# Optimization experiments

Hardware: AMD Instinct MI355X
Metric: run time of the kernel (lower is better)

The kernel has to match this reference:

```python
import jax, jax.numpy as jnp
import numpy as np
import math

SAMPLING_FACTOR = 5


def setup_inputs() -> dict:
    key = jax.random.key(0)
    kq, kk, kv, ki = jax.random.split(key, 4)
    B, L_Q, L_K, d = 8, 4096, 4096, 64
    # U_part = min(5 * L_Q * ceil(log1p(L_K)), L_K) = 4096 for these sizes
    U_part = min(SAMPLING_FACTOR * L_Q * math.ceil(math.log1p(L_K)), L_K)
    q = jax.random.normal(kq, (B, L_Q, d), dtype=jnp.float32)
    K = jax.random.normal(kk, (B, L_K, d), dtype=jnp.float32)
    V = jax.random.normal(kv, (B, L_K, d), dtype=jnp.float32)
    index_sample = jax.random.randint(ki, (U_part,), 0, L_K)  # random key sample (torch.randint)
    return {"q": q, "K": K, "V": V, "index_sample": index_sample}


def reference(q, K, V, index_sample):
    B, L_Q, d = q.shape
    L_K = K.shape[1]
    log_L_Q = math.ceil(math.log1p(L_Q))
    u = min(SAMPLING_FACTOR * log_L_Q, L_Q)  # number of selected queries (45 here)

    # Random key sampling (indices shared across batch)
    K_sample = K[:, index_sample, :]                       # [B, U_part, d]
    # Q @ K_sample^T
    Q_K_sample = jnp.einsum('bqd,bud->bqu', q, K_sample)   # [B, L_Q, U_part]
    # Sparsity measure M = max - sum/L_K
    M = Q_K_sample.max(axis=-1) - Q_K_sample.sum(axis=-1) / L_K  # [B, L_Q]
    # Source uses topk(..., largest=False): pick queries with SMALLEST M (kept faithfully)
    _, M_top = jax.lax.top_k(-M, u)                        # [B, u]
    # Gather the selected queries
    Q_reduce = jnp.take_along_axis(q, M_top[:, :, None], axis=1)  # [B, u, d]
    # Full attention over all keys for the selected queries
    attn_scores = jnp.einsum('bud,bkd->buk', Q_reduce, K) / math.sqrt(d)  # [B, u, L_K]
    attn_probs = jax.nn.softmax(attn_scores, axis=-1)
    attn_output = jnp.einsum('buk,bkd->bud', attn_probs, V)  # [B, u, d]
    return attn_output, attn_scores
```

## Files before the change

kernel.cpp:

```cpp
#include <hip/hip_runtime.h>
#include <hip/hip_bf16.h>
#include <math.h>

#define BB 8
#define LQ 4096
#define LK 4096
#define DD 64
#define UU 45
#define CCAP 256
#define CUMTHR 96
#define ECH 32
#define PCH 32
#define MCG 4
#define GCH 32

typedef __bf16 bf16x8 __attribute__((ext_vector_type(8)));
typedef unsigned short ushort8 __attribute__((ext_vector_type(8)));
typedef float f32x4 __attribute__((ext_vector_type(4)));

__device__ inline unsigned short f2bf(float x) {
    unsigned u = __builtin_bit_cast(unsigned, x);
    return (unsigned short)((u + 0x7FFF + ((u >> 16) & 1)) >> 16);
}

__device__ inline void gl_lds16(const void* g, void* l) {
    __builtin_amdgcn_global_load_lds(
        (const __attribute__((address_space(1))) unsigned int*)g,
        (__attribute__((address_space(3))) unsigned int*)l, 16, 0, 0);
}

__global__ __launch_bounds__(256) void k_gatherK(const float* __restrict__ K,
                                                 const int* __restrict__ idx,
                                                 int Upart,
                                                 unsigned short* __restrict__ Kg,
                                                 double* __restrict__ part) {
    int b = blockIdx.y;
    int chunk = blockIdx.x;
    int u0 = chunk * 128;
    int t = threadIdx.x;
    int pt = t & 7;

    double acc[8] = {0,0,0,0,0,0,0,0};
    #pragma unroll
    for (int i = 0; i < 4; ++i) {
        int lin = i * 256 + t;
        int u = u0 + (lin >> 3);
        if (u < Upart) {
            int kr = idx[u];
            const float* src = &K[((size_t)b * LK + kr) * DD + pt * 8];
            float4 v0 = *(const float4*)src;
            float4 v1 = *(const float4*)(src + 4);
            ushort8 pk;
            pk[0]=f2bf(v0.x); pk[1]=f2bf(v0.y); pk[2]=f2bf(v0.z); pk[3]=f2bf(v0.w);
            pk[4]=f2bf(v1.x); pk[5]=f2bf(v1.y); pk[6]=f2bf(v1.z); pk[7]=f2bf(v1.w);
            *(ushort8*)&Kg[((size_t)b * 4096 + u) * 64 + pt * 8] = pk;
            acc[0] += (double)v0.x; acc[1] += (double)v0.y;
            acc[2] += (double)v0.z; acc[3] += (double)v0.w;
            acc[4] += (double)v1.x; acc[5] += (double)v1.y;
            acc[6] += (double)v1.z; acc[7] += (double)v1.w;
        }
    }
    __shared__ double sred[32][64];
    int rg = t >> 3;
    #pragma unroll
    for (int j = 0; j < 8; ++j) sred[rg][pt * 8 + j] = acc[j];
    __syncthreads();
    if (t < 64) {
        double s = 0.0;
        #pragma unroll
        for (int r = 0; r < 32; ++r) s += sred[r][t];
        part[((size_t)(b * GCH + chunk)) * 64 + t] = s;
    }
}

__global__ __launch_bounds__(256) void k_mfmaM(const float* __restrict__ Q,
                                               const unsigned short* __restrict__ Kg,
                                               float* __restrict__ maxpart) {
    int bx = blockIdx.x, cg = blockIdx.y, b = blockIdx.z;
    int t = threadIdx.x;
    int lane = t & 63, w = t >> 6;
    int row0 = bx * 256;

    __shared__ unsigned short smem[16384];

    for (int i = 0; i < 8; ++i) {
        int u = i * 256 + t;
        int r = u >> 3, s = u & 7;
        int c = s ^ (r & 7);
        const float* src = &Q[((size_t)b * LQ + row0 + r) * DD + c * 8];
        float4 v0 = *(const float4*)src;
        float4 v1 = *(const float4*)(src + 4);
        ushort8 pk;
        pk[0]=f2bf(v0.x); pk[1]=f2bf(v0.y); pk[2]=f2bf(v0.z); pk[3]=f2bf(v0.w);
        pk[4]=f2bf(v1.x); pk[5]=f2bf(v1.y); pk[6]=f2bf(v1.z); pk[7]=f2bf(v1.w);
        *(ushort8*)&smem[r * 64 + s * 8] = pk;
    }
    __syncthreads();

    bf16x8 afr[4][2];
    #pragma unroll
    for (int rf = 0; rf < 4; ++rf)
        #pragma unroll
        for (int kh = 0; kh < 2; ++kh) {
            int r = w * 64 + rf * 16 + (lane & 15);
            int slot = (kh * 4 + (lane >> 4)) ^ (r & 7);
            afr[rf][kh] = __builtin_bit_cast(bf16x8, *(const ushort8*)&smem[r * 64 + slot * 8]);
        }
    __syncthreads();

    int krl = lane >> 3;
    int kc8 = (lane & 7) ^ (krl & 7);
    const unsigned short* kgb = Kg + ((size_t)b * 4096 + cg * 1024) * 64;

    #define STAGE_K(buf, tile)                                                  \
        {                                                                       \
            _Pragma("unroll")                                                   \
            for (int i_ = 0; i_ < 4; ++i_) {                                    \
                int seg_ = w * 4 + i_;                                          \
                const unsigned short* g_ =                                      \
                    kgb + ((size_t)((tile) * 128 + seg_ * 8 + krl)) * 64 + kc8 * 8; \
                gl_lds16(g_, &smem[(buf) * 8192 + seg_ * 512]);                 \
            }                                                                   \
        }

    STAGE_K(0, 0)
    __syncthreads();

    float rowmax[4][4];
    #pragma unroll
    for (int rf = 0; rf < 4; ++rf)
        #pragma unroll
        for (int g = 0; g < 4; ++g) rowmax[rf][g] = -INFINITY;

    for (int tile = 0; tile < 8; ++tile) {
        int cur = tile & 1;
        if (tile < 7) STAGE_K(cur ^ 1, tile + 1)

        #pragma unroll
        for (int cf = 0; cf < 8; ++cf) {
            f32x4 acc[4];
            #pragma unroll
            for (int rf = 0; rf < 4; ++rf) acc[rf] = (f32x4){0.f, 0.f, 0.f, 0.f};
            #pragma unroll
            for (int kh = 0; kh < 2; ++kh) {
                int ccol = cf * 16 + (lane & 15);
                int slot = (kh * 4 + (lane >> 4)) ^ (ccol & 7);
                bf16x8 bfr = __builtin_bit_cast(bf16x8,
                    *(const ushort8*)&smem[cur * 8192 + ccol * 64 + slot * 8]);
                #pragma unroll
                for (int rf = 0; rf < 4; ++rf)
                    acc[rf] = __builtin_amdgcn_mfma_f32_16x16x32_bf16(afr[rf][kh], bfr, acc[rf], 0, 0, 0);
            }
            #pragma unroll
            for (int rf = 0; rf < 4; ++rf)
                #pragma unroll
                for (int g = 0; g < 4; ++g)
                    rowmax[rf][g] = fmaxf(rowmax[rf][g], acc[rf][g]);
        }
        __syncthreads();
    }

    #pragma unroll
    for (int rf = 0; rf < 4; ++rf)
        #pragma unroll
        for (int g = 0; g < 4; ++g) {
            float m = rowmax[rf][g];
            m = fmaxf(m, __shfl_xor(m, 1));
            m = fmaxf(m, __shfl_xor(m, 2));
            m = fmaxf(m, __shfl_xor(m, 4));
            m = fmaxf(m, __shfl_xor(m, 8));
            if ((lane & 15) == 0) {
                int row = row0 + w * 64 + rf * 16 + (lane >> 4) * 4 + g;
                maxpart[((size_t)(b * MCG + cg)) * LQ + row] = m;
            }
        }
}

__global__ __launch_bounds__(256) void k_meanmerge(const float* __restrict__ Q,
                                                   const double* __restrict__ part,
                                                   int nch,
                                                   const float* __restrict__ maxpart,
                                                   double* __restrict__ mt,
                                                   float* __restrict__ Map) {
    int b = blockIdx.y;
    int t = threadIdx.x;
    int r = blockIdx.x * 256 + t;
    __shared__ double sK[64];
    if (t < 64) {
        double s = 0.0;
        for (int ch = 0; ch < nch; ++ch)
            s += part[((size_t)(b * GCH + ch)) * 64 + t];
        sK[t] = s;
    }
    __syncthreads();
    const float* qr = &Q[((size_t)b * LQ + r) * DD];
    double a0 = 0, a1 = 0, a2 = 0, a3 = 0;
    #pragma unroll
    for (int d = 0; d < 64; d += 4) {
        a0 += (double)qr[d + 0] * sK[d + 0];
        a1 += (double)qr[d + 1] * sK[d + 1];
        a2 += (double)qr[d + 2] * sK[d + 2];
        a3 += (double)qr[d + 3] * sK[d + 3];
    }
    double m = ((a0 + a1) + (a2 + a3)) / (double)LK;
    mt[(size_t)b * LQ + r] = m;
    float mx = fmaxf(fmaxf(maxpart[((size_t)(b * MCG + 0)) * LQ + r],
                           maxpart[((size_t)(b * MCG + 1)) * LQ + r]),
                     fmaxf(maxpart[((size_t)(b * MCG + 2)) * LQ + r],
                           maxpart[((size_t)(b * MCG + 3)) * LQ + r]));
    Map[(size_t)b * LQ + r] = mx - (float)m;
}

__global__ __launch_bounds__(1024) void k_select(const float* __restrict__ Map,
                                                 int* __restrict__ cand,
                                                 int* __restrict__ cand_count) {
    int b = blockIdx.x;
    int t = threadIdx.x;
    __shared__ float mv[LQ];
    __shared__ int hist[1024];
    __shared__ int seg[256];
    __shared__ float wmin[16], wmax[16];
    __shared__ float s_min, s_max;
    __shared__ int s_bstar, s_cnt;

    float lmin = INFINITY, lmax = -INFINITY;
    for (int i = t; i < LQ; i += 1024) {
        float v = Map[(size_t)b * LQ + i];
        mv[i] = v;
        lmin = fminf(lmin, v);
        lmax = fmaxf(lmax, v);
    }
    #pragma unroll
    for (int m = 1; m < 64; m <<= 1) {
        lmin = fminf(lmin, __shfl_xor(lmin, m));
        lmax = fmaxf(lmax, __shfl_xor(lmax, m));
    }
    int wid = t >> 6;
    if ((t & 63) == 0) { wmin[wid] = lmin; wmax[wid] = lmax; }
    if (t < 1024) hist[t] = 0;
    __syncthreads();
    if (t == 0) {
        float mn = wmin[0], mx = wmax[0];
        #pragma unroll
        for (int i = 1; i < 16; ++i) { mn = fminf(mn, wmin[i]); mx = fmaxf(mx, wmax[i]); }
        s_min = mn; s_max = mx;
        s_cnt = 0;
        s_bstar = 1023;
    }
    __syncthreads();
    float vmin = s_min;
    float w = (s_max - vmin) * (1.0f / 1024.0f);
    if (w <= 0.f) w = 1e-30f;
    float inv = 1.0f / w;
    for (int i = t; i < LQ; i += 1024) {
        int bin = (int)((mv[i] - vmin) * inv);
        bin = min(max(bin, 0), 1023);
        atomicAdd(&hist[bin], 1);
    }
    __syncthreads();
    int h0 = 0, h1 = 0, h2 = 0, h3 = 0;
    if (t < 256) {
        h0 = hist[t * 4 + 0]; h1 = hist[t * 4 + 1];
        h2 = hist[t * 4 + 2]; h3 = hist[t * 4 + 3];
        seg[t] = h0 + h1 + h2 + h3;
    }
    __syncthreads();
    for (int off = 1; off < 256; off <<= 1) {
        int v = 0, add = 0;
        if (t < 256) { v = seg[t]; add = (t >= off) ? seg[t - off] : 0; }
        __syncthreads();
        if (t < 256) seg[t] = v + add;
        __syncthreads();
    }
    if (t < 256) {
        int prev = (t == 0) ? 0 : seg[t - 1];
        if (seg[t] >= CUMTHR && prev < CUMTHR) {
            int cum = prev, bs = t * 4 + 3;
            if (cum + h0 >= CUMTHR) bs = t * 4;
            else if (cum + h0 + h1 >= CUMTHR) bs = t * 4 + 1;
            else if (cum + h0 + h1 + h2 >= CUMTHR) bs = t * 4 + 2;
            s_bstar = bs;
        }
    }
    __syncthreads();
    int bstar = s_bstar;
    for (int i = t; i < LQ; i += 1024) {
        int bin = (int)((mv[i] - vmin) * inv);
        bin = min(max(bin, 0), 1023);
        if (bin <= bstar) {
            int p = atomicAdd(&s_cnt, 1);
            if (p < CCAP) cand[b * CCAP + p] = i;
        }
    }
    __syncthreads();
    if (t == 0) cand_count[b] = min(s_cnt, CCAP);
}

__global__ __launch_bounds__(256, 1) void k_exact(const float* __restrict__ Q,
                                                  const float* __restrict__ K,
                                                  const int* __restrict__ idx,
                                                  const int* __restrict__ cand,
                                                  const int* __restrict__ cand_count,
                                                  float* __restrict__ exactpart) {
    int kc = blockIdx.x;
    int b  = blockIdx.y;
    int t = threadIdx.x;
    int lane = t & 63, w = t >> 6;
    __shared__ float Ks[128 * 64];
    __shared__ float wmx[4][CCAP];

    #pragma unroll
    for (int p = 0; p < 8; ++p) {
        int row = p * 16 + (t >> 4);
        int c4 = t & 15;
        int kr = idx[kc * 128 + row];
        *(float4*)&Ks[row * 64 + c4 * 4] =
            *(const float4*)&K[((size_t)b * LK + kr) * DD + c4 * 4];
    }

    int count = cand_count[b];
    int npass = (count + 127) >> 7;
    __syncthreads();

    for (int pass = 0; pass < npass; ++pass) {
        int s0 = pass * 128 + lane;
        int s1 = s0 + 64;
        float4 q0[16], q1[16];
        {
            float4 z = {0.f, 0.f, 0.f, 0.f};
            if (s0 < count) {
                const float4* qp = (const float4*)&Q[((size_t)b * LQ + cand[b * CCAP + s0]) * DD];
                #pragma unroll
                for (int i = 0; i < 16; ++i) q0[i] = qp[i];
            } else {
                #pragma unroll
                for (int i = 0; i < 16; ++i) q0[i] = z;
            }
            if (s1 < count) {
                const float4* qp = (const float4*)&Q[((size_t)b * LQ + cand[b * CCAP + s1]) * DD];
                #pragma unroll
                for (int i = 0; i < 16; ++i) q1[i] = qp[i];
            } else {
                #pragma unroll
                for (int i = 0; i < 16; ++i) q1[i] = z;
            }
        }

        float m0 = -INFINITY, m1 = -INFINITY;
        int kbeg = w * 32;
        for (int k = kbeg; k < kbeg + 32; ++k) {
            const float4* kr4 = (const float4*)&Ks[k * 64];
            float a0=0.f,a1=0.f,a2=0.f,a3=0.f;
            float c0=0.f,c1=0.f,c2=0.f,c3=0.f;
            #pragma unroll
            for (int i = 0; i < 16; i += 4) {
                float4 kv0 = kr4[i+0], kv1 = kr4[i+1], kv2 = kr4[i+2], kv3 = kr4[i+3];
                a0 = fmaf(q0[i+0].x, kv0.x, a0); a0 = fmaf(q0[i+0].y, kv0.y, a0);
                a0 = fmaf(q0[i+0].z, kv0.z, a0); a0 = fmaf(q0[i+0].w, kv0.w, a0);
                a1 = fmaf(q0[i+1].x, kv1.x, a1); a1 = fmaf(q0[i+1].y, kv1.y, a1);
                a1 = fmaf(q0[i+1].z, kv1.z, a1); a1 = fmaf(q0[i+1].w, kv1.w, a1);
                a2 = fmaf(q0[i+2].x, kv2.x, a2); a2 = fmaf(q0[i+2].y, kv2.y, a2);
                a2 = fmaf(q0[i+2].z, kv2.z, a2); a2 = fmaf(q0[i+2].w, kv2.w, a2);
                a3 = fmaf(q0[i+3].x, kv3.x, a3); a3 = fmaf(q0[i+3].y, kv3.y, a3);
                a3 = fmaf(q0[i+3].z, kv3.z, a3); a3 = fmaf(q0[i+3].w, kv3.w, a3);
                c0 = fmaf(q1[i+0].x, kv0.x, c0); c0 = fmaf(q1[i+0].y, kv0.y, c0);
                c0 = fmaf(q1[i+0].z, kv0.z, c0); c0 = fmaf(q1[i+0].w, kv0.w, c0);
                c1 = fmaf(q1[i+1].x, kv1.x, c1); c1 = fmaf(q1[i+1].y, kv1.y, c1);
                c1 = fmaf(q1[i+1].z, kv1.z, c1); c1 = fmaf(q1[i+1].w, kv1.w, c1);
                c2 = fmaf(q1[i+2].x, kv2.x, c2); c2 = fmaf(q1[i+2].y, kv2.y, c2);
                c2 = fmaf(q1[i+2].z, kv2.z, c2); c2 = fmaf(q1[i+2].w, kv2.w, c2);
                c3 = fmaf(q1[i+3].x, kv3.x, c3); c3 = fmaf(q1[i+3].y, kv3.y, c3);
                c3 = fmaf(q1[i+3].z, kv3.z, c3); c3 = fmaf(q1[i+3].w, kv3.w, c3);
            }
            m0 = fmaxf(m0, (a0 + a1) + (a2 + a3));
            m1 = fmaxf(m1, (c0 + c1) + (c2 + c3));
        }
        wmx[w][s0] = m0;
        if (s1 < CCAP) wmx[w][s1] = m1;
    }
    __syncthreads();

    if (t < count) {
        float m = fmaxf(fmaxf(wmx[0][t], wmx[1][t]), fmaxf(wmx[2][t], wmx[3][t]));
        exactpart[((size_t)(b * CCAP + t)) * ECH + kc] = m;
    }
}

__global__ __launch_bounds__(64) void k_final45(const float* __restrict__ exactpart,
                                                const double* __restrict__ mt,
                                                const int* __restrict__ cand,
                                                const int* __restrict__ cand_count,
                                                int* __restrict__ Mtop) {
    int b = blockIdx.x;
    int l = threadIdx.x;
    int count = cand_count[b];
    float val[4];
    int oid[4];
    #pragma unroll
    for (int j = 0; j < 4; ++j) {
        int slot = l + j * 64;
        if (slot < count) {
            const float* ep = &exactpart[((size_t)(b * CCAP + slot)) * ECH];
            float m = ep[0];
            #pragma unroll
            for (int k = 1; k < ECH; ++k) m = fmaxf(m, ep[k]);
            int r = cand[b * CCAP + slot];
            val[j] = m - (float)mt[(size_t)b * LQ + r];
            oid[j] = r;
        } else { val[j] = INFINITY; oid[j] = 0x7FFFFFFF; }
    }
    for (int it = 0; it < UU; ++it) {
        float bv = val[0]; int bi = oid[0], bj = 0;
        #pragma unroll
        for (int j = 1; j < 4; ++j)
            if (val[j] < bv || (val[j] == bv && oid[j] < bi)) { bv = val[j]; bi = oid[j]; bj = j; }
        float rv = bv; int ri = bi;
        #pragma unroll
        for (int m = 1; m < 64; m <<= 1) {
            float ov = __shfl_xor(rv, m);
            int oi = __shfl_xor(ri, m);
            if (ov < rv || (ov == rv && oi < ri)) { rv = ov; ri = oi; }
        }
        if (l == 0) Mtop[b * UU + it] = ri;
        if (rv == bv && ri == bi) val[bj] = INFINITY;
    }
}

__global__ __launch_bounds__(256) void k_spv(const float* __restrict__ Q,
                                             const float* __restrict__ K,
                                             const float* __restrict__ V,
                                             const int* __restrict__ Mtop,
                                             float* __restrict__ scores,
                                             float2* __restrict__ stats,
                                             float* __restrict__ partial) {
    int ch = blockIdx.x, b = blockIdx.y;
    int t = threadIdx.x;
    int lane = t & 63, w = t >> 6;
    int k0 = ch * 128;

    __shared__ float Qs[48][64];
    __shared__ float Vs[128 * 64];
    __shared__ float Ps[48][128];
    __shared__ float2 st[48];

    for (int i = t; i < 48 * 64; i += 256) {
        int r = i >> 6, dd = i & 63;
        Qs[r][dd] = (r < UU) ? Q[((size_t)b * LQ + Mtop[b * UU + r]) * DD + dd] : 0.f;
    }
    for (int p = 0; p < 8; ++p) {
        int lin = p * 1024 + t * 4;
        *(float4*)&Vs[lin] = *(const float4*)&V[((size_t)b * LK + k0) * DD + lin];
    }
    __syncthreads();

    {
        int key = t & 127;
        int rh = t >> 7;
        int r0 = rh * 23;
        int r1 = rh ? UU : 23;
        const float* Krow = &K[((size_t)(b * LK + k0 + key)) * DD];
        float4 kv[16];
        #pragma unroll
        for (int i = 0; i < 16; ++i) kv[i] = ((const float4*)Krow)[i];
        for (int r = r0; r < r1; ++r) {
            const float4* qr = (const float4*)&Qs[r][0];
            float d0 = 0.f, d1 = 0.f, d2 = 0.f, d3 = 0.f;
            #pragma unroll
            for (int i = 0; i < 16; i += 4) {
                float4 q0 = qr[i+0], q1 = qr[i+1], q2 = qr[i+2], q3 = qr[i+3];
                d0 = fmaf(q0.x, kv[i+0].x, d0); d0 = fmaf(q0.y, kv[i+0].y, d0);
                d0 = fmaf(q0.z, kv[i+0].z, d0); d0 = fmaf(q0.w, kv[i+0].w, d0);
                d1 = fmaf(q1.x, kv[i+1].x, d1); d1 = fmaf(q1.y, kv[i+1].y, d1);
                d1 = fmaf(q1.z, kv[i+1].z, d1); d1 = fmaf(q1.w, kv[i+1].w, d1);
                d2 = fmaf(q2.x, kv[i+2].x, d2); d2 = fmaf(q2.y, kv[i+2].y, d2);
                d2 = fmaf(q2.z, kv[i+2].z, d2); d2 = fmaf(q2.w, kv[i+2].w, d2);
                d3 = fmaf(q3.x, kv[i+3].x, d3); d3 = fmaf(q3.y, kv[i+3].y, d3);
                d3 = fmaf(q3.z, kv[i+3].z, d3); d3 = fmaf(q3.w, kv[i+3].w, d3);
            }
            float sc = ((d0 + d1) + (d2 + d3)) * 0.125f;
            Ps[r][key] = sc;
            scores[((size_t)(b * UU + r)) * LK + k0 + key] = sc;
        }
    }
    __syncthreads();

    for (int r = w; r < 48; r += 4) {
        if (r < UU) {
            float v0 = Ps[r][lane], v1 = Ps[r][lane + 64];
            float m = fmaxf(v0, v1);
            #pragma unroll
            for (int o = 32; o; o >>= 1) m = fmaxf(m, __shfl_xor(m, o));
            float e0 = __expf(v0 - m), e1 = __expf(v1 - m);
            float s = e0 + e1;
            #pragma unroll
            for (int o = 32; o; o >>= 1) s += __shfl_xor(s, o);
            Ps[r][lane] = e0; Ps[r][lane + 64] = e1;
            if (lane == 0) st[r] = make_float2(m, s);
        } else {
            Ps[r][lane] = 0.f; Ps[r][lane + 64] = 0.f;
        }
    }
    __syncthreads();

    {
        int d = t & 63, rg = t >> 6;
        float acc[12];
        #pragma unroll
        for (int i = 0; i < 12; ++i) acc[i] = 0.f;
        for (int k = 0; k < 128; ++k) {
            float vv = Vs[k * 64 + d];
            #pragma unroll
            for (int i = 0; i < 12; ++i)
                acc[i] += Ps[rg * 12 + i][k] * vv;
        }
        #pragma unroll
        for (int i = 0; i < 12; ++i) {
            int r = rg * 12 + i;
            if (r < UU)
                partial[(((size_t)(b * PCH + ch)) * UU + r) * 64 + d] = acc[i];
        }
    }
    if (t < UU) stats[((size_t)(b * PCH + ch)) * UU + t] = st[t];
}

__global__ __launch_bounds__(256) void k_combine(const float* __restrict__ partial,
                                                 const float2* __restrict__ stats,
                                                 float* __restrict__ out) {
    int b = blockIdx.x;
    int t = threadIdx.x;
    __shared__ float wgt[UU][PCH];
    if (t < UU) {
        float mx[PCH], sm[PCH];
        #pragma unroll
        for (int c = 0; c < PCH; ++c) {
            float2 v = stats[((size_t)(b * PCH + c)) * UU + t];
            mx[c] = v.x; sm[c] = v.y;
        }
        float m = mx[0];
        #pragma unroll
        for (int c = 1; c < PCH; ++c) m = fmaxf(m, mx[c]);
        float S = 0.f;
        #pragma unroll
        for (int c = 0; c < PCH; ++c) {
            float e = __expf(mx[c] - m);
            wgt[t][c] = e;
            S += sm[c] * e;
        }
        float inv = 1.0f / S;
        #pragma unroll
        for (int c = 0; c < PCH; ++c) wgt[t][c] *= inv;
    }
    __syncthreads();
    for (int o = t; o < UU * 64; o += 256) {
        int r = o >> 6, d = o & 63;
        float s = 0.f;
        #pragma unroll 8
        for (int c = 0; c < PCH; ++c)
            s += partial[(((size_t)(b * PCH + c)) * UU + r) * 64 + d] * wgt[r][c];
        out[((size_t)(b * UU + r)) * 64 + d] = s;
    }
}

extern "C" void kernel_launch(void* const* d_in, const int* in_sizes, int n_in,
                              void* d_out, int out_size, void* d_ws, size_t ws_size,
                              hipStream_t stream) {
    const float* q   = (const float*)d_in[0];
    const float* K   = (const float*)d_in[1];
    const float* V   = (const float*)d_in[2];
    const int*   idx = (const int*)d_in[3];
    int Upart = in_sizes[3];
    int nch = (Upart + 127) / 128;

    char* ws = (char*)d_ws;
    size_t off = 0;
    unsigned short* Kg = (unsigned short*)(ws + off); off += (size_t)BB * 4096 * 64 * 2;
    float*  maxpart   = (float*)(ws + off);  off += (size_t)BB * MCG * LQ * 4;
    double* mt        = (double*)(ws + off); off += (size_t)BB * LQ * 8;
    float*  Map       = (float*)(ws + off);  off += (size_t)BB * LQ * 4;
    int*    cand      = (int*)(ws + off);    off += (size_t)BB * CCAP * 4;
    int*    cand_cnt  = (int*)(ws + off);    off += 256;
    int*    Mtop      = (int*)(ws + off);    off += 2048;
    float2* stats     = (float2*)(ws + off); off += (size_t)BB * PCH * UU * 8 + 256;
    float*  partial   = (float*)(ws + off);  off += (size_t)BB * PCH * UU * 64 * 4;
    double* sumKpart  = (double*)partial;
    float*  exactpart = (float*)partial;

    float* out_attn   = (float*)d_out;
    float* out_scores = out_attn + BB * UU * 64;

    k_gatherK  <<<dim3(nch, BB), 256, 0, stream>>>(K, idx, Upart, Kg, sumKpart);
    k_mfmaM    <<<dim3(LQ / 256, MCG, BB), 256, 0, stream>>>(q, Kg, maxpart);
    k_meanmerge<<<dim3(LQ / 256, BB), 256, 0, stream>>>(q, sumKpart, nch, maxpart, mt, Map);
    k_select   <<<dim3(BB), 1024, 0, stream>>>(Map, cand, cand_cnt);
    k_exact    <<<dim3(ECH, BB), 256, 0, stream>>>(q, K, idx, cand, cand_cnt, exactpart);
    k_final45  <<<dim3(BB), 64, 0, stream>>>(exactpart, mt, cand, cand_cnt, Mtop);
    k_spv      <<<dim3(PCH, BB), 256, 0, stream>>>(q, K, V, Mtop, out_scores, stats, partial);
    k_combine  <<<dim3(BB), 256, 0, stream>>>(partial, stats, out_attn);
}
```

Before: 151.3 us.

## Double grid parallelism across mfmaM, exact, spv, and split combine over d

Doubles the number of key chunks for the max-M MFMA kernel (MCG 4→8), the exact candidate scoring kernel (ECH 32→64) and the softmax·V kernel (PCH 32→64), halving per-block work so more CUs are busy on a 256-CU part. The combine kernel is also split across four d-quarters per batch, and its stats loops are no longer unrolled into register arrays. The cost is more partial results to merge (more exactpart/stats/partial traffic and longer reduction loops) and smaller per-block tiles with less reuse.

```diff
diff --git a/kernel.cpp b/kernel.cpp
--- a/kernel.cpp
+++ b/kernel.cpp
@@ -9,9 +9,9 @@
 #define UU 45
 #define CCAP 256
 #define CUMTHR 96
-#define ECH 32
-#define PCH 32
-#define MCG 4
+#define ECH 64
+#define PCH 64
+#define MCG 8
 #define GCH 32
 
 typedef __bf16 bf16x8 __attribute__((ext_vector_type(8)));
@@ -110,7 +110,7 @@
 
     int krl = lane >> 3;
     int kc8 = (lane & 7) ^ (krl & 7);
-    const unsigned short* kgb = Kg + ((size_t)b * 4096 + cg * 1024) * 64;
+    const unsigned short* kgb = Kg + ((size_t)b * 4096 + cg * 512) * 64;
 
     #define STAGE_K(buf, tile)                                                  \
         {                                                                       \
@@ -132,9 +132,9 @@
         #pragma unroll
         for (int g = 0; g < 4; ++g) rowmax[rf][g] = -INFINITY;
 
-    for (int tile = 0; tile < 8; ++tile) {
+    for (int tile = 0; tile < 4; ++tile) {
         int cur = tile & 1;
-        if (tile < 7) STAGE_K(cur ^ 1, tile + 1)
+        if (tile < 3) STAGE_K(cur ^ 1, tile + 1)
 
         #pragma unroll
         for (int cf = 0; cf < 8; ++cf) {
@@ -204,10 +204,10 @@
     }
     double m = ((a0 + a1) + (a2 + a3)) / (double)LK;
     mt[(size_t)b * LQ + r] = m;
-    float mx = fmaxf(fmaxf(maxpart[((size_t)(b * MCG + 0)) * LQ + r],
-                           maxpart[((size_t)(b * MCG + 1)) * LQ + r]),
-                     fmaxf(maxpart[((size_t)(b * MCG + 2)) * LQ + r],
-                           maxpart[((size_t)(b * MCG + 3)) * LQ + r]));
+    float mx = -INFINITY;
+    #pragma unroll
+    for (int g = 0; g < MCG; ++g)
+        mx = fmaxf(mx, maxpart[((size_t)(b * MCG + g)) * LQ + r]);
     Map[(size_t)b * LQ + r] = mx - (float)m;
 }
 
@@ -296,24 +296,24 @@
     if (t == 0) cand_count[b] = min(s_cnt, CCAP);
 }
 
-__global__ __launch_bounds__(256, 1) void k_exact(const float* __restrict__ Q,
-                                                  const float* __restrict__ K,
-                                                  const int* __restrict__ idx,
-                                                  const int* __restrict__ cand,
-                                                  const int* __restrict__ cand_count,
-                                                  float* __restrict__ exactpart) {
+__global__ __launch_bounds__(256) void k_exact(const float* __restrict__ Q,
+                                               const float* __restrict__ K,
+                                               const int* __restrict__ idx,
+                                               const int* __restrict__ cand,
+                                               const int* __restrict__ cand_count,
+                                               float* __restrict__ exactpart) {
     int kc = blockIdx.x;
     int b  = blockIdx.y;
     int t = threadIdx.x;
     int lane = t & 63, w = t >> 6;
-    __shared__ float Ks[128 * 64];
+    __shared__ float Ks[64 * 64];
     __shared__ float wmx[4][CCAP];
 
     #pragma unroll
-    for (int p = 0; p < 8; ++p) {
+    for (int p = 0; p < 4; ++p) {
         int row = p * 16 + (t >> 4);
         int c4 = t & 15;
-        int kr = idx[kc * 128 + row];
+        int kr = idx[kc * 64 + row];
         *(float4*)&Ks[row * 64 + c4 * 4] =
             *(const float4*)&K[((size_t)b * LK + kr) * DD + c4 * 4];
     }
@@ -347,8 +347,8 @@
         }
 
         float m0 = -INFINITY, m1 = -INFINITY;
-        int kbeg = w * 32;
-        for (int k = kbeg; k < kbeg + 32; ++k) {
+        int kbeg = w * 16;
+        for (int k = kbeg; k < kbeg + 16; ++k) {
             const float4* kr4 = (const float4*)&Ks[k * 64];
             float a0=0.f,a1=0.f,a2=0.f,a3=0.f;
             float c0=0.f,c1=0.f,c2=0.f,c3=0.f;
@@ -400,10 +400,13 @@
     for (int j = 0; j < 4; ++j) {
         int slot = l + j * 64;
         if (slot < count) {
-            const float* ep = &exactpart[((size_t)(b * CCAP + slot)) * ECH];
-            float m = ep[0];
-            #pragma unroll
-            for (int k = 1; k < ECH; ++k) m = fmaxf(m, ep[k]);
+            const float4* ep = (const float4*)&exactpart[((size_t)(b * CCAP + slot)) * ECH];
+            float m = -INFINITY;
+            #pragma unroll
+            for (int k = 0; k < ECH / 4; ++k) {
+                float4 v = ep[k];
+                m = fmaxf(m, fmaxf(fmaxf(v.x, v.y), fmaxf(v.z, v.w)));
+            }
             int r = cand[b * CCAP + slot];
             val[j] = m - (float)mt[(size_t)b * LQ + r];
             oid[j] = r;
@@ -436,28 +439,28 @@
     int ch = blockIdx.x, b = blockIdx.y;
     int t = threadIdx.x;
     int lane = t & 63, w = t >> 6;
-    int k0 = ch * 128;
+    int k0 = ch * 64;
 
     __shared__ float Qs[48][64];
-    __shared__ float Vs[128 * 64];
-    __shared__ float Ps[48][128];
+    __shared__ float Vs[64 * 64];
+    __shared__ float Ps[48][64];
     __shared__ float2 st[48];
 
     for (int i = t; i < 48 * 64; i += 256) {
         int r = i >> 6, dd = i & 63;
         Qs[r][dd] = (r < UU) ? Q[((size_t)b * LQ + Mtop[b * UU + r]) * DD + dd] : 0.f;
     }
-    for (int p = 0; p < 8; ++p) {
+    for (int p = 0; p < 4; ++p) {
         int lin = p * 1024 + t * 4;
         *(float4*)&Vs[lin] = *(const float4*)&V[((size_t)b * LK + k0) * DD + lin];
     }
     __syncthreads();
 
     {
-        int key = t & 127;
-        int rh = t >> 7;
-        int r0 = rh * 23;
-        int r1 = rh ? UU : 23;
+        int key = t & 63;
+        int rq = t >> 6;
+        int r0 = rq * 12;
+        int r1 = min(r0 + 12, UU);
         const float* Krow = &K[((size_t)(b * LK + k0 + key)) * DD];
         float4 kv[16];
         #pragma unroll
@@ -486,18 +489,18 @@
 
     for (int r = w; r < 48; r += 4) {
         if (r < UU) {
-            float v0 = Ps[r][lane], v1 = Ps[r][lane + 64];
-            float m = fmaxf(v0, v1);
+            float v = Ps[r][lane];
+            float m = v;
             #pragma unroll
             for (int o = 32; o; o >>= 1) m = fmaxf(m, __shfl_xor(m, o));
-            float e0 = __expf(v0 - m), e1 = __expf(v1 - m);
-            float s = e0 + e1;
+            float e = __expf(v - m);
+            float s = e;
             #pragma unroll
             for (int o = 32; o; o >>= 1) s += __shfl_xor(s, o);
-            Ps[r][lane] = e0; Ps[r][lane + 64] = e1;
+            Ps[r][lane] = e;
             if (lane == 0) st[r] = make_float2(m, s);
         } else {
-            Ps[r][lane] = 0.f; Ps[r][lane + 64] = 0.f;
+            Ps[r][lane] = 0.f;
         }
     }
     __syncthreads();
@@ -507,7 +510,7 @@
         float acc[12];
         #pragma unroll
         for (int i = 0; i < 12; ++i) acc[i] = 0.f;
-        for (int k = 0; k < 128; ++k) {
+        for (int k = 0; k < 64; ++k) {
             float vv = Vs[k * 64 + d];
             #pragma unroll
             for (int i = 0; i < 12; ++i)
@@ -526,33 +529,28 @@
 __global__ __launch_bounds__(256) void k_combine(const float* __restrict__ partial,
                                                  const float2* __restrict__ stats,
                                                  float* __restrict__ out) {
-    int b = blockIdx.x;
+    int dq = blockIdx.x;
+    int b = blockIdx.y;
     int t = threadIdx.x;
     __shared__ float wgt[UU][PCH];
     if (t < UU) {
-        float mx[PCH], sm[PCH];
-        #pragma unroll
+        float m = -INFINITY;
+        for (int c = 0; c < PCH; ++c)
+            m = fmaxf(m, stats[((size_t)(b * PCH + c)) * UU + t].x);
+        float S = 0.f;
         for (int c = 0; c < PCH; ++c) {
             float2 v = stats[((size_t)(b * PCH + c)) * UU + t];
-            mx[c] = v.x; sm[c] = v.y;
-        }
-        float m = mx[0];
-        #pragma unroll
-        for (int c = 1; c < PCH; ++c) m = fmaxf(m, mx[c]);
-        float S = 0.f;
-        #pragma unroll
-        for (int c = 0; c < PCH; ++c) {
-            float e = __expf(mx[c] - m);
+            float e = __expf(v.x - m);
             wgt[t][c] = e;
-            S += sm[c] * e;
+            S += v.y * e;
         }
         float inv = 1.0f / S;
-        #pragma unroll
         for (int c = 0; c < PCH; ++c) wgt[t][c] *= inv;
     }
     __syncthreads();
-    for (int o = t; o < UU * 64; o += 256) {
-        int r = o >> 6, d = o & 63;
+    for (int o = t; o < UU * 16; o += 256) {
+        int r = o >> 4;
+        int d = dq * 16 + (o & 15);
         float s = 0.f;
         #pragma unroll 8
         for (int c = 0; c < PCH; ++c)
@@ -595,5 +593,5 @@
     k_exact    <<<dim3(ECH, BB), 256, 0, stream>>>(q, K, idx, cand, cand_cnt, exactpart);
     k_final45  <<<dim3(BB), 64, 0, stream>>>(exactpart, mt, cand, cand_cnt, Mtop);
     k_spv      <<<dim3(PCH, BB), 256, 0, stream>>>(q, K, V, Mtop, out_scores, stats, partial);
-    k_combine  <<<dim3(BB), 256, 0, stream>>>(partial, stats, out_attn);
-}
+    k_combine  <<<dim3(4, BB), 256, 0, stream>>>(partial, stats, out_attn);
+}
```

Result: no change. 153.8 us (+1.7%).

## Deduplicate sampled key indices before max-score GEMM and exact rescoring

Applied to the files above, without the earlier changes.

Builds a per-batch bitmap of the sampled key indices with atomics and compacts them into a unique list, since randint sampling repeats many indices and the row max does not depend on duplicates. A new gather kernel converts only the unique keys to bf16, and the MFMA max kernel and exact rescoring kernel skip tiles past the unique count. The column sum still uses every sample. This adds a zeroing kernel, an extra gather launch and atomic contention in exchange for less GEMM work. Unique-list order is nondeterministic, but the max is order-independent.

```diff
diff --git a/kernel.cpp b/kernel.cpp
--- a/kernel.cpp
+++ b/kernel.cpp
@@ -29,10 +29,17 @@
         (__attribute__((address_space(3))) unsigned int*)l, 16, 0, 0);
 }
 
+__global__ __launch_bounds__(1024) void k_zero(unsigned int* __restrict__ bm) {
+    int t = blockIdx.x * 1024 + threadIdx.x;
+    if (t < BB * 128 + BB) bm[t] = 0;
+}
+
 __global__ __launch_bounds__(256) void k_gatherK(const float* __restrict__ K,
                                                  const int* __restrict__ idx,
                                                  int Upart,
-                                                 unsigned short* __restrict__ Kg,
+                                                 unsigned int* __restrict__ bm,
+                                                 unsigned int* __restrict__ ucnt,
+                                                 int* __restrict__ uniq,
                                                  double* __restrict__ part) {
     int b = blockIdx.y;
     int chunk = blockIdx.x;
@@ -47,13 +54,17 @@
         int u = u0 + (lin >> 3);
         if (u < Upart) {
             int kr = idx[u];
+            if (pt == 0) {
+                unsigned bit = 1u << (kr & 31);
+                unsigned old = atomicOr(&bm[b * 128 + (kr >> 5)], bit);
+                if (!(old & bit)) {
+                    unsigned p = atomicAdd(&ucnt[b], 1u);
+                    uniq[b * 4096 + p] = kr;
+                }
+            }
             const float* src = &K[((size_t)b * LK + kr) * DD + pt * 8];
             float4 v0 = *(const float4*)src;
             float4 v1 = *(const float4*)(src + 4);
-            ushort8 pk;
-            pk[0]=f2bf(v0.x); pk[1]=f2bf(v0.y); pk[2]=f2bf(v0.z); pk[3]=f2bf(v0.w);
-            pk[4]=f2bf(v1.x); pk[5]=f2bf(v1.y); pk[6]=f2bf(v1.z); pk[7]=f2bf(v1.w);
-            *(ushort8*)&Kg[((size_t)b * 4096 + u) * 64 + pt * 8] = pk;
             acc[0] += (double)v0.x; acc[1] += (double)v0.y;
             acc[2] += (double)v0.z; acc[3] += (double)v0.w;
             acc[4] += (double)v1.x; acc[5] += (double)v1.y;
@@ -73,13 +84,57 @@
     }
 }
 
+__global__ __launch_bounds__(256) void k_gatherKu(const float* __restrict__ K,
+                                                  const unsigned int* __restrict__ ucnt,
+                                                  const int* __restrict__ uniq,
+                                                  unsigned short* __restrict__ Kgu) {
+    int b = blockIdx.y;
+    int chunk = blockIdx.x;
+    int count = (int)ucnt[b];
+    int padded = (count + 127) & ~127;
+    if (chunk * 128 >= padded) return;
+    int t = threadIdx.x;
+    int pt = t & 7;
+    #pragma unroll
+    for (int i = 0; i < 4; ++i) {
+        int lin = i * 256 + t;
+        int u = chunk * 128 + (lin >> 3);
+        int kr = uniq[b * 4096 + ((u < count) ? u : 0)];
+        const float* src = &K[((size_t)b * LK + kr) * DD + pt * 8];
+        float4 v0 = *(const float4*)src;
+        float4 v1 = *(const float4*)(src + 4);
+        ushort8 pk;
+        pk[0]=f2bf(v0.x); pk[1]=f2bf(v0.y); pk[2]=f2bf(v0.z); pk[3]=f2bf(v0.w);
+        pk[4]=f2bf(v1.x); pk[5]=f2bf(v1.y); pk[6]=f2bf(v1.z); pk[7]=f2bf(v1.w);
+        *(ushort8*)&Kgu[((size_t)b * 4096 + u) * 64 + pt * 8] = pk;
+    }
+}
+
 __global__ __launch_bounds__(256) void k_mfmaM(const float* __restrict__ Q,
-                                               const unsigned short* __restrict__ Kg,
+                                               const unsigned short* __restrict__ Kgu,
+                                               const unsigned int* __restrict__ ucnt,
                                                float* __restrict__ maxpart) {
     int bx = blockIdx.x, cg = blockIdx.y, b = blockIdx.z;
     int t = threadIdx.x;
     int lane = t & 63, w = t >> 6;
     int row0 = bx * 256;
+
+    int padded = ((int)ucnt[b] + 127) & ~127;
+    int tiles_total = padded >> 7;
+    int nt = tiles_total - cg * 8;
+    if (nt > 8) nt = 8;
+
+    if (nt <= 0) {
+        #pragma unroll
+        for (int rf = 0; rf < 4; ++rf)
+            #pragma unroll
+            for (int g = 0; g < 4; ++g)
+                if ((lane & 15) == 0) {
+                    int row = row0 + w * 64 + rf * 16 + (lane >> 4) * 4 + g;
+                    maxpart[((size_t)(b * MCG + cg)) * LQ + row] = -INFINITY;
+                }
+        return;
+    }
 
     __shared__ unsigned short smem[16384];
 
@@ -110,7 +165,7 @@
 
     int krl = lane >> 3;
     int kc8 = (lane & 7) ^ (krl & 7);
-    const unsigned short* kgb = Kg + ((size_t)b * 4096 + cg * 1024) * 64;
+    const unsigned short* kgb = Kgu + ((size_t)b * 4096 + cg * 1024) * 64;
 
     #define STAGE_K(buf, tile)                                                  \
         {                                                                       \
@@ -132,9 +187,9 @@
         #pragma unroll
         for (int g = 0; g < 4; ++g) rowmax[rf][g] = -INFINITY;
 
-    for (int tile = 0; tile < 8; ++tile) {
+    for (int tile = 0; tile < nt; ++tile) {
         int cur = tile & 1;
-        if (tile < 7) STAGE_K(cur ^ 1, tile + 1)
+        if (tile + 1 < nt) STAGE_K(cur ^ 1, tile + 1)
 
         #pragma unroll
         for (int cf = 0; cf < 8; ++cf) {
@@ -204,10 +259,10 @@
     }
     double m = ((a0 + a1) + (a2 + a3)) / (double)LK;
     mt[(size_t)b * LQ + r] = m;
-    float mx = fmaxf(fmaxf(maxpart[((size_t)(b * MCG + 0)) * LQ + r],
-                           maxpart[((size_t)(b * MCG + 1)) * LQ + r]),
-                     fmaxf(maxpart[((size_t)(b * MCG + 2)) * LQ + r],
-                           maxpart[((size_t)(b * MCG + 3)) * LQ + r]));
+    float mx = -INFINITY;
+    #pragma unroll
+    for (int g = 0; g < MCG; ++g)
+        mx = fmaxf(mx, maxpart[((size_t)(b * MCG + g)) * LQ + r]);
     Map[(size_t)b * LQ + r] = mx - (float)m;
 }
 
@@ -298,13 +353,22 @@
 
 __global__ __launch_bounds__(256, 1) void k_exact(const float* __restrict__ Q,
                                                   const float* __restrict__ K,
-                                                  const int* __restrict__ idx,
+                                                  const unsigned int* __restrict__ ucnt,
+                                                  const int* __restrict__ uniq,
                                                   const int* __restrict__ cand,
                                                   const int* __restrict__ cand_count,
                                                   float* __restrict__ exactpart) {
     int kc = blockIdx.x;
     int b  = blockIdx.y;
     int t = threadIdx.x;
+    int count = cand_count[b];
+    int ucount = (int)ucnt[b];
+    int padded = (ucount + 127) & ~127;
+    if (kc * 128 >= padded) {
+        if (t < count)
+            exactpart[((size_t)(b * CCAP + t)) * ECH + kc] = -INFINITY;
+        return;
+    }
     int lane = t & 63, w = t >> 6;
     __shared__ float Ks[128 * 64];
     __shared__ float wmx[4][CCAP];
@@ -313,12 +377,12 @@
     for (int p = 0; p < 8; ++p) {
         int row = p * 16 + (t >> 4);
         int c4 = t & 15;
-        int kr = idx[kc * 128 + row];
+        int ui = kc * 128 + row;
+        int kr = uniq[b * 4096 + ((ui < ucount) ? ui : 0)];
         *(float4*)&Ks[row * 64 + c4 * 4] =
             *(const float4*)&K[((size_t)b * LK + kr) * DD + c4 * 4];
     }
 
-    int count = cand_count[b];
     int npass = (count + 127) >> 7;
     __syncthreads();
 
@@ -400,10 +464,13 @@
     for (int j = 0; j < 4; ++j) {
         int slot = l + j * 64;
         if (slot < count) {
-            const float* ep = &exactpart[((size_t)(b * CCAP + slot)) * ECH];
-            float m = ep[0];
-            #pragma unroll
-            for (int k = 1; k < ECH; ++k) m = fmaxf(m, ep[k]);
+            const float4* ep = (const float4*)&exactpart[((size_t)(b * CCAP + slot)) * ECH];
+            float m = -INFINITY;
+            #pragma unroll
+            for (int k = 0; k < ECH / 4; ++k) {
+                float4 v = ep[k];
+                m = fmaxf(m, fmaxf(fmaxf(v.x, v.y), fmaxf(v.z, v.w)));
+            }
             int r = cand[b * CCAP + slot];
             val[j] = m - (float)mt[(size_t)b * LQ + r];
             oid[j] = r;
@@ -573,7 +640,10 @@
 
     char* ws = (char*)d_ws;
     size_t off = 0;
-    unsigned short* Kg = (unsigned short*)(ws + off); off += (size_t)BB * 4096 * 64 * 2;
+    unsigned short* Kgu = (unsigned short*)(ws + off); off += (size_t)BB * 4096 * 64 * 2;
+    unsigned int* bm   = (unsigned int*)(ws + off);   off += (size_t)BB * 128 * 4;
+    unsigned int* ucnt = (unsigned int*)(ws + off);   off += 256;
+    int*    uniq      = (int*)(ws + off);    off += (size_t)BB * 4096 * 4;
     float*  maxpart   = (float*)(ws + off);  off += (size_t)BB * MCG * LQ * 4;
     double* mt        = (double*)(ws + off); off += (size_t)BB * LQ * 8;
     float*  Map       = (float*)(ws + off);  off += (size_t)BB * LQ * 4;
@@ -588,11 +658,13 @@
     float* out_attn   = (float*)d_out;
     float* out_scores = out_attn + BB * UU * 64;
 
-    k_gatherK  <<<dim3(nch, BB), 256, 0, stream>>>(K, idx, Upart, Kg, sumKpart);
-    k_mfmaM    <<<dim3(LQ / 256, MCG, BB), 256, 0, stream>>>(q, Kg, maxpart);
+    k_zero     <<<dim3(2), 1024, 0, stream>>>(bm);
+    k_gatherK  <<<dim3(nch, BB), 256, 0, stream>>>(K, idx, Upart, bm, ucnt, uniq, sumKpart);
+    k_gatherKu <<<dim3(32, BB), 256, 0, stream>>>(K, ucnt, uniq, Kgu);
+    k_mfmaM    <<<dim3(LQ / 256, MCG, BB), 256, 0, stream>>>(q, Kgu, ucnt, maxpart);
     k_meanmerge<<<dim3(LQ / 256, BB), 256, 0, stream>>>(q, sumKpart, nch, maxpart, mt, Map);
     k_select   <<<dim3(BB), 1024, 0, stream>>>(Map, cand, cand_cnt);
-    k_exact    <<<dim3(ECH, BB), 256, 0, stream>>>(q, K, idx, cand, cand_cnt, exactpart);
+    k_exact    <<<dim3(ECH, BB), 256, 0, stream>>>(q, K, ucnt, uniq, cand, cand_cnt, exactpart);
     k_final45  <<<dim3(BB), 64, 0, stream>>>(exactpart, mt, cand, cand_cnt, Mtop);
     k_spv      <<<dim3(PCH, BB), 256, 0, stream>>>(q, K, V, Mtop, out_scores, stats, partial);
     k_combine  <<<dim3(BB), 256, 0, stream>>>(partial, stats, out_attn);
```

Result: slower. 203.0 us (+34.2%).
